# Performance work log

Hardware: AMD Instinct MI355X
Metric: run time of the kernel (lower is better)

The kernel has to match this reference:

```python
import jax, jax.numpy as jnp
import numpy as np
import itertools

FIELD_NUM = 24

def _pair_idx(field_num):
    pairs = np.array(list(itertools.combinations(range(field_num), 2)), dtype=np.int32)
    return pairs[:, 0], pairs[:, 1]

def setup_inputs() -> dict:
    key = jax.random.key(0)
    k1, k2 = jax.random.split(key)
    B, F, E = 4096, FIELD_NUM, 64
    P = F * (F - 1) // 2  # 276
    x = jax.random.normal(k1, (B, F, E), dtype=jnp.float32)
    W = jax.random.normal(k2, (P, E, E), dtype=jnp.float32) * 0.05
    return {"x": x, "W": W}

def reference(x, W):
    # x: [B, F, E]; W: [P, E, E] one weight per field pair (field_interaction)
    i_idx, j_idx = _pair_idx(x.shape[1])
    xi = x[:, i_idx, :]  # [B, P, E]
    xj = x[:, j_idx, :]  # [B, P, E]
    # per-pair bilinear transform then Hadamard product; concat over pair axis
    return jnp.einsum('bpe,pef->bpf', xi, W) * xj  # [B, P, E]
```

## Files before the change

### kernel.cpp

```cpp
#include <hip/hip_runtime.h>

typedef short s16x8 __attribute__((ext_vector_type(8)));
typedef float f32x4 __attribute__((ext_vector_type(4)));

constexpr int F  = 24;
constexpr int NP = 276;
constexpr int E  = 64;

__device__ __forceinline__ unsigned short f2bf(float f) {
    unsigned int u = __builtin_bit_cast(unsigned int, f);
    return (unsigned short)((u + 0x7FFFu + ((u >> 16) & 1u)) >> 16);
}

__global__ __launch_bounds__(256)
void bilinear_kernel(const float* __restrict__ x, const float* __restrict__ W,
                     float* __restrict__ out)
{
    __shared__ unsigned int BtU[2048];

    const int bid = blockIdx.x;
    const int xcd = bid & 7;
    const int idx = bid >> 3;
    const int wl  = (idx >= NP) ? 1 : 0;
    const int p   = idx - wl * NP;
    const int b0  = (xcd * 2 + wl) * 256;

    const int tid = threadIdx.x;
    const int wv  = tid >> 6;
    const int ln  = tid & 63;

    int i = 0, rem = p;
    while (rem >= F - 1 - i) { rem -= F - 1 - i; ++i; }
    const int j = i + 1 + rem;

    const float* Wp = W + (size_t)p * E * E;
    #pragma unroll
    for (int it = 0; it < 8; ++it) {
        int q  = tid + it * 256;
        int f  = q & 63;
        int e2 = q >> 6;
        float w0 = Wp[(2 * e2) * E + f];
        float w1 = Wp[(2 * e2 + 1) * E + f];
        unsigned int pk = (unsigned int)f2bf(w0) | ((unsigned int)f2bf(w1) << 16);
        BtU[f * 32 + (e2 ^ ((f & 7) << 2))] = pk;
    }
    __syncthreads();

    const unsigned short* Bts = reinterpret_cast<const unsigned short*>(BtU);

    const int lrow = ln & 15;
    const int lq   = ln >> 4;

    s16x8 bfrag[4][2];
    #pragma unroll
    for (int n = 0; n < 4; ++n) {
        int fc = n * 16 + lrow;
        #pragma unroll
        for (int kk = 0; kk < 2; ++kk) {
            int k0 = kk * 32 + lq * 8;
            int sidx = fc * 64 + (k0 ^ ((fc & 7) << 3));
            bfrag[n][kk] = *reinterpret_cast<const s16x8*>(&Bts[sidx]);
        }
    }

    #pragma unroll 1
    for (int s = 0; s < 4; ++s) {
        const int mbase = s * 64 + wv * 16;

        s16x8 afrag[2];
        #pragma unroll
        for (int kk = 0; kk < 2; ++kk) {
            int b  = b0 + mbase + lrow;
            int k0 = kk * 32 + lq * 8;
            const float4* ap = reinterpret_cast<const float4*>(
                x + ((size_t)b * F + i) * E + k0);
            float4 lo = ap[0], hi = ap[1];
            s16x8 a;
            a[0] = (short)f2bf(lo.x); a[1] = (short)f2bf(lo.y);
            a[2] = (short)f2bf(lo.z); a[3] = (short)f2bf(lo.w);
            a[4] = (short)f2bf(hi.x); a[5] = (short)f2bf(hi.y);
            a[6] = (short)f2bf(hi.z); a[7] = (short)f2bf(hi.w);
            afrag[kk] = a;
        }

        f32x4 acc[4];
        #pragma unroll
        for (int n = 0; n < 4; ++n) {
            acc[n] = (f32x4){0.f, 0.f, 0.f, 0.f};
            acc[n] = __builtin_amdgcn_mfma_f32_16x16x32_bf16(afrag[0], bfrag[n][0], acc[n], 0, 0, 0);
            acc[n] = __builtin_amdgcn_mfma_f32_16x16x32_bf16(afrag[1], bfrag[n][1], acc[n], 0, 0, 0);
        }

        #pragma unroll
        for (int n = 0; n < 4; ++n) {
            int fc = n * 16 + lrow;
            #pragma unroll
            for (int r = 0; r < 4; ++r) {
                int m = mbase + lq * 4 + r;
                int b = b0 + m;
                float xj = x[((size_t)b * F + j) * E + fc];
                out[((size_t)b * NP + p) * E + fc] = acc[n][r] * xj;
            }
        }
    }
}

extern "C" void kernel_launch(void* const* d_in, const int* in_sizes, int n_in,
                              void* d_out, int out_size, void* d_ws, size_t ws_size,
                              hipStream_t stream)
{
    const float* x = (const float*)d_in[0];
    const float* W = (const float*)d_in[1];
    float* out = (float*)d_out;
    dim3 grid(NP * 16, 1, 1);
    bilinear_kernel<<<grid, 256, 0, stream>>>(x, W, out);
}
```

Measured before the change: 83.16 us.

## Retile over pair chunks and stage output in LDS for wide coalesced stores

Each block now covers 64 batch rows and 4 consecutive pairs instead of 256 rows and one pair. Results for the 4 pairs are staged in a padded shared buffer and then written as contiguous 1 KB rows with 16-byte vector stores. Before, each store was a scattered 4-byte write. The cost is reloading and converting each W matrix many more times (once per 64 rows instead of once per 256), extra barriers, and about 66 KB of LDS per block, which may lower occupancy.

```diff
diff --git a/kernel.cpp b/kernel.cpp
--- a/kernel.cpp
+++ b/kernel.cpp
@@ -6,6 +6,9 @@
 constexpr int F  = 24;
 constexpr int NP = 276;
 constexpr int E  = 64;
+constexpr int CH = 4;
+constexpr int NB = 64;
+constexpr int OS = 260;
 
 __device__ __forceinline__ unsigned short f2bf(float f) {
     unsigned int u = __builtin_bit_cast(unsigned int, f);
@@ -17,64 +20,67 @@
                      float* __restrict__ out)
 {
     __shared__ unsigned int BtU[2048];
+    __shared__ float Obuf[NB * OS];
 
     const int bid = blockIdx.x;
     const int xcd = bid & 7;
-    const int idx = bid >> 3;
-    const int wl  = (idx >= NP) ? 1 : 0;
-    const int p   = idx - wl * NP;
-    const int b0  = (xcd * 2 + wl) * 256;
+    const int l   = bid >> 3;
+    const int bb  = xcd * 8 + l / 69;
+    const int ch  = l % 69;
+    const int b0  = bb * NB;
+    const int p0  = ch * CH;
 
-    const int tid = threadIdx.x;
-    const int wv  = tid >> 6;
-    const int ln  = tid & 63;
-
-    int i = 0, rem = p;
-    while (rem >= F - 1 - i) { rem -= F - 1 - i; ++i; }
-    const int j = i + 1 + rem;
-
-    const float* Wp = W + (size_t)p * E * E;
-    #pragma unroll
-    for (int it = 0; it < 8; ++it) {
-        int q  = tid + it * 256;
-        int f  = q & 63;
-        int e2 = q >> 6;
-        float w0 = Wp[(2 * e2) * E + f];
-        float w1 = Wp[(2 * e2 + 1) * E + f];
-        unsigned int pk = (unsigned int)f2bf(w0) | ((unsigned int)f2bf(w1) << 16);
-        BtU[f * 32 + (e2 ^ ((f & 7) << 2))] = pk;
-    }
-    __syncthreads();
-
-    const unsigned short* Bts = reinterpret_cast<const unsigned short*>(BtU);
-
+    const int tid  = threadIdx.x;
+    const int wv   = tid >> 6;
+    const int ln   = tid & 63;
     const int lrow = ln & 15;
     const int lq   = ln >> 4;
 
-    s16x8 bfrag[4][2];
-    #pragma unroll
-    for (int n = 0; n < 4; ++n) {
-        int fc = n * 16 + lrow;
+    #pragma unroll 1
+    for (int pp = 0; pp < CH; ++pp) {
+        const int p = p0 + pp;
+
+        int i = 0, rem = p;
+        while (rem >= F - 1 - i) { rem -= F - 1 - i; ++i; }
+        const int j = i + 1 + rem;
+
+        if (pp) __syncthreads();
+
+        const float* Wp = W + (size_t)p * E * E;
+        #pragma unroll
+        for (int it = 0; it < 8; ++it) {
+            int q  = tid + it * 256;
+            int f  = q & 63;
+            int e2 = q >> 6;
+            float w0 = Wp[(2 * e2) * E + f];
+            float w1 = Wp[(2 * e2 + 1) * E + f];
+            unsigned int pk = (unsigned int)f2bf(w0) | ((unsigned int)f2bf(w1) << 16);
+            BtU[f * 32 + (e2 ^ ((f & 7) << 2))] = pk;
+        }
+        __syncthreads();
+
+        const unsigned short* Bts = reinterpret_cast<const unsigned short*>(BtU);
+
+        s16x8 bfrag[4][2];
+        #pragma unroll
+        for (int n = 0; n < 4; ++n) {
+            int fc = n * 16 + lrow;
+            #pragma unroll
+            for (int kk = 0; kk < 2; ++kk) {
+                int k0 = kk * 32 + lq * 8;
+                int sidx = fc * 64 + (k0 ^ ((fc & 7) << 3));
+                bfrag[n][kk] = *reinterpret_cast<const s16x8*>(&Bts[sidx]);
+            }
+        }
+
+        const int bA = b0 + wv * 16 + lrow;
+        const float* xi_ = x + ((size_t)bA * F + i) * E;
+        s16x8 afrag[2];
         #pragma unroll
         for (int kk = 0; kk < 2; ++kk) {
             int k0 = kk * 32 + lq * 8;
-            int sidx = fc * 64 + (k0 ^ ((fc & 7) << 3));
-            bfrag[n][kk] = *reinterpret_cast<const s16x8*>(&Bts[sidx]);
-        }
-    }
-
-    #pragma unroll 1
-    for (int s = 0; s < 4; ++s) {
-        const int mbase = s * 64 + wv * 16;
-
-        s16x8 afrag[2];
-        #pragma unroll
-        for (int kk = 0; kk < 2; ++kk) {
-            int b  = b0 + mbase + lrow;
-            int k0 = kk * 32 + lq * 8;
-            const float4* ap = reinterpret_cast<const float4*>(
-                x + ((size_t)b * F + i) * E + k0);
-            float4 lo = ap[0], hi = ap[1];
+            float4 lo = *reinterpret_cast<const float4*>(xi_ + k0);
+            float4 hi = *reinterpret_cast<const float4*>(xi_ + k0 + 4);
             s16x8 a;
             a[0] = (short)f2bf(lo.x); a[1] = (short)f2bf(lo.y);
             a[2] = (short)f2bf(lo.z); a[3] = (short)f2bf(lo.w);
@@ -96,12 +102,19 @@
             int fc = n * 16 + lrow;
             #pragma unroll
             for (int r = 0; r < 4; ++r) {
-                int m = mbase + lq * 4 + r;
-                int b = b0 + m;
-                float xj = x[((size_t)b * F + j) * E + fc];
-                out[((size_t)b * NP + p) * E + fc] = acc[n][r] * xj;
+                int row = wv * 16 + lq * 4 + r;
+                float xj = x[((size_t)(b0 + row) * F + j) * E + fc];
+                Obuf[row * OS + pp * 64 + fc] = acc[n][r] * xj;
             }
         }
+    }
+
+    #pragma unroll
+    for (int rr = 0; rr < 16; ++rr) {
+        const int row = wv * 16 + rr;
+        const f32x4 v = *reinterpret_cast<const f32x4*>(&Obuf[row * OS + ln * 4]);
+        float* op = out + ((size_t)(b0 + row) * NP + p0) * E + ln * 4;
+        *reinterpret_cast<f32x4*>(op) = v;
     }
 }
 
@@ -112,6 +125,6 @@
     const float* x = (const float*)d_in[0];
     const float* W = (const float*)d_in[1];
     float* out = (float*)d_out;
-    dim3 grid(NP * 16, 1, 1);
+    dim3 grid(64 * 69, 1, 1);
     bilinear_kernel<<<grid, 256, 0, stream>>>(x, W, out);
 }
```

Measured after the change: 113.2 us. 36.2% more time.

## Process two adjacent field pairs per block and use nontemporal output stores

Applied to the files above, without the earlier changes.

Each block now handles two consecutive pairs (p0, p0+1), so the grid is halved. Both W matrices are staged in LDS and the two MFMA chains are interleaved, and the two output rows written per batch element are adjacent, which gives more contiguous writes. Output stores become nontemporal to avoid polluting cache with the large output stream. The cost is double the LDS and fragment registers per block, which may reduce occupancy, and there are fewer blocks to spread across CUs.

```diff
diff --git a/kernel.cpp b/kernel.cpp
--- a/kernel.cpp
+++ b/kernel.cpp
@@ -16,79 +16,97 @@
 void bilinear_kernel(const float* __restrict__ x, const float* __restrict__ W,
                      float* __restrict__ out)
 {
-    __shared__ unsigned int BtU[2048];
+    __shared__ unsigned int BtU[2][2048];
 
     const int bid = blockIdx.x;
     const int xcd = bid & 7;
     const int idx = bid >> 3;
-    const int wl  = (idx >= NP) ? 1 : 0;
-    const int p   = idx - wl * NP;
+    const int wl  = (idx >= 138) ? 1 : 0;
+    const int ck  = idx - wl * 138;
     const int b0  = (xcd * 2 + wl) * 256;
+    const int p0  = ck * 2;
 
-    const int tid = threadIdx.x;
-    const int wv  = tid >> 6;
-    const int ln  = tid & 63;
+    const int tid  = threadIdx.x;
+    const int wv   = tid >> 6;
+    const int ln   = tid & 63;
+    const int lrow = ln & 15;
+    const int lq   = ln >> 4;
 
-    int i = 0, rem = p;
-    while (rem >= F - 1 - i) { rem -= F - 1 - i; ++i; }
-    const int j = i + 1 + rem;
+    int i0 = 0, rem = p0;
+    while (rem >= F - 1 - i0) { rem -= F - 1 - i0; ++i0; }
+    const int j0 = i0 + 1 + rem;
+    int i1 = i0, j1 = j0 + 1;
+    if (j1 == F) { i1 = i0 + 1; j1 = i1 + 1; }
 
-    const float* Wp = W + (size_t)p * E * E;
     #pragma unroll
-    for (int it = 0; it < 8; ++it) {
-        int q  = tid + it * 256;
-        int f  = q & 63;
-        int e2 = q >> 6;
-        float w0 = Wp[(2 * e2) * E + f];
-        float w1 = Wp[(2 * e2 + 1) * E + f];
-        unsigned int pk = (unsigned int)f2bf(w0) | ((unsigned int)f2bf(w1) << 16);
-        BtU[f * 32 + (e2 ^ ((f & 7) << 2))] = pk;
+    for (int pr = 0; pr < 2; ++pr) {
+        const float* Wp = W + (size_t)(p0 + pr) * E * E;
+        #pragma unroll
+        for (int it = 0; it < 8; ++it) {
+            int q  = tid + it * 256;
+            int f  = q & 63;
+            int e2 = q >> 6;
+            float w0 = Wp[(2 * e2) * E + f];
+            float w1 = Wp[(2 * e2 + 1) * E + f];
+            unsigned int pk = (unsigned int)f2bf(w0) | ((unsigned int)f2bf(w1) << 16);
+            BtU[pr][f * 32 + (e2 ^ ((f & 7) << 2))] = pk;
+        }
     }
     __syncthreads();
 
-    const unsigned short* Bts = reinterpret_cast<const unsigned short*>(BtU);
-
-    const int lrow = ln & 15;
-    const int lq   = ln >> 4;
-
-    s16x8 bfrag[4][2];
+    s16x8 bfrag[2][4][2];
     #pragma unroll
-    for (int n = 0; n < 4; ++n) {
-        int fc = n * 16 + lrow;
+    for (int pr = 0; pr < 2; ++pr) {
+        const unsigned short* Bts = reinterpret_cast<const unsigned short*>(BtU[pr]);
         #pragma unroll
-        for (int kk = 0; kk < 2; ++kk) {
-            int k0 = kk * 32 + lq * 8;
-            int sidx = fc * 64 + (k0 ^ ((fc & 7) << 3));
-            bfrag[n][kk] = *reinterpret_cast<const s16x8*>(&Bts[sidx]);
+        for (int n = 0; n < 4; ++n) {
+            int fc = n * 16 + lrow;
+            #pragma unroll
+            for (int kk = 0; kk < 2; ++kk) {
+                int k0 = kk * 32 + lq * 8;
+                int sidx = fc * 64 + (k0 ^ ((fc & 7) << 3));
+                bfrag[pr][n][kk] = *reinterpret_cast<const s16x8*>(&Bts[sidx]);
+            }
         }
     }
 
     #pragma unroll 1
     for (int s = 0; s < 4; ++s) {
         const int mbase = s * 64 + wv * 16;
+        const int bA = b0 + mbase + lrow;
 
-        s16x8 afrag[2];
+        s16x8 af0[2], af1[2];
         #pragma unroll
         for (int kk = 0; kk < 2; ++kk) {
-            int b  = b0 + mbase + lrow;
             int k0 = kk * 32 + lq * 8;
-            const float4* ap = reinterpret_cast<const float4*>(
-                x + ((size_t)b * F + i) * E + k0);
-            float4 lo = ap[0], hi = ap[1];
+            const float4* ap0 = reinterpret_cast<const float4*>(
+                x + ((size_t)bA * F + i0) * E + k0);
+            float4 lo = ap0[0], hi = ap0[1];
             s16x8 a;
             a[0] = (short)f2bf(lo.x); a[1] = (short)f2bf(lo.y);
             a[2] = (short)f2bf(lo.z); a[3] = (short)f2bf(lo.w);
             a[4] = (short)f2bf(hi.x); a[5] = (short)f2bf(hi.y);
             a[6] = (short)f2bf(hi.z); a[7] = (short)f2bf(hi.w);
-            afrag[kk] = a;
+            af0[kk] = a;
+            const float4* ap1 = reinterpret_cast<const float4*>(
+                x + ((size_t)bA * F + i1) * E + k0);
+            lo = ap1[0]; hi = ap1[1];
+            a[0] = (short)f2bf(lo.x); a[1] = (short)f2bf(lo.y);
+            a[2] = (short)f2bf(lo.z); a[3] = (short)f2bf(lo.w);
+            a[4] = (short)f2bf(hi.x); a[5] = (short)f2bf(hi.y);
+            a[6] = (short)f2bf(hi.z); a[7] = (short)f2bf(hi.w);
+            af1[kk] = a;
         }
 
-        f32x4 acc[4];
+        f32x4 acc0[4], acc1[4];
         #pragma unroll
         for (int n = 0; n < 4; ++n) {
-            acc[n] = (f32x4){0.f, 0.f, 0.f, 0.f};
-            acc[n] = __builtin_amdgcn_mfma_f32_16x16x32_bf16(afrag[0], bfrag[n][0], acc[n], 0, 0, 0);
-            acc[n] = __builtin_amdgcn_mfma_f32_16x16x32_bf16(afrag[1], bfrag[n][1], acc[n], 0, 0, 0);
+            acc0[n] = (f32x4){0.f, 0.f, 0.f, 0.f};
+            acc0[n] = __builtin_amdgcn_mfma_f32_16x16x32_bf16(af0[0], bfrag[0][n][0], acc0[n], 0, 0, 0);
+            acc0[n] = __builtin_amdgcn_mfma_f32_16x16x32_bf16(af0[1], bfrag[0][n][1], acc0[n], 0, 0, 0);
+            acc1[n] = (f32x4){0.f, 0.f, 0.f, 0.f};
+            acc1[n] = __builtin_amdgcn_mfma_f32_16x16x32_bf16(af1[0], bfrag[1][n][0], acc1[n], 0, 0, 0);
+            acc1[n] = __builtin_amdgcn_mfma_f32_16x16x32_bf16(af1[1], bfrag[1][n][1], acc1[n], 0, 0, 0);
         }
 
         #pragma unroll
@@ -96,10 +114,12 @@
             int fc = n * 16 + lrow;
             #pragma unroll
             for (int r = 0; r < 4; ++r) {
-                int m = mbase + lq * 4 + r;
-                int b = b0 + m;
-                float xj = x[((size_t)b * F + j) * E + fc];
-                out[((size_t)b * NP + p) * E + fc] = acc[n][r] * xj;
+                int b = b0 + mbase + lq * 4 + r;
+                float xj0 = x[((size_t)b * F + j0) * E + fc];
+                float xj1 = x[((size_t)b * F + j1) * E + fc];
+                float* op = out + ((size_t)b * NP + p0) * E + fc;
+                __builtin_nontemporal_store(acc0[n][r] * xj0, op);
+                __builtin_nontemporal_store(acc1[n][r] * xj1, op + E);
             }
         }
     }
@@ -112,6 +132,6 @@
     const float* x = (const float*)d_in[0];
     const float* W = (const float*)d_in[1];
     float* out = (float*)d_out;
-    dim3 grid(NP * 16, 1, 1);
+    dim3 grid(138 * 16, 1, 1);
     bilinear_kernel<<<grid, 256, 0, stream>>>(x, W, out);
 }
```

Result: faster. 74.49 us (-10.4%).
